# Kernel optimization log

Hardware: AMD Instinct MI355X
Metric: run time of the kernel (lower is better)

The kernel has to match this reference:

```python
import jax, jax.numpy as jnp
import numpy as np
from jax import lax

SOS_TOKEN = 0
PAD_LEN = 30  # tokenizer.pad_len -> number of greedy decode steps


def _gru_cell(x, h, w_ih, w_hh, b_ih, b_hh):
    # PyTorch GRU cell math. x,h: [B,H]; w_*: [3H,H]; b_*: [3H]
    gi = x @ w_ih.T + b_ih
    gh = h @ w_hh.T + b_hh
    i_r, i_z, i_n = jnp.split(gi, 3, axis=-1)
    h_r, h_z, h_n = jnp.split(gh, 3, axis=-1)
    r = jax.nn.sigmoid(i_r + h_r)
    z = jax.nn.sigmoid(i_z + h_z)
    n = jnp.tanh(i_n + r * h_n)
    return (1.0 - z) * n + z * h


def _sm_encode(sm_hidden, conv_w, conv_b, enc_w, enc_b):
    # sm_hidden: [B, L, C] -> conv over time with C input channels
    x = jnp.transpose(sm_hidden, (0, 2, 1))  # [B, C, L]
    conv = lax.conv_general_dilated(
        x, conv_w, window_strides=(1,), padding='VALID',
        dimension_numbers=('NCH', 'OIH', 'NCH'))  # [B, O, L-k+1]
    conv = jax.nn.relu(conv + conv_b[None, :, None])
    pooled = jnp.max(conv, axis=-1)  # [B, O]
    return jax.nn.relu(pooled @ enc_w.T + enc_b)  # [B, H]


def reference(sm_hidden, embedding, w_ih, w_hh, b_ih, b_hh,
              w_out, b_out, conv_w, conv_b, enc_w, enc_b):
    B = sm_hidden.shape[0]
    h0 = _sm_encode(sm_hidden, conv_w, conv_b, enc_w, enc_b)  # [B, H]

    # The original re-runs the GRU over the whole (append-only) prefix each
    # iteration; since the GRU is deterministic this equals incremental
    # single-step updates, which we do here.
    def step(carry, _):
        h, tok = carry
        emb = embedding[tok]                      # [B, H]
        h_new = _gru_cell(emb, h, w_ih, w_hh, b_ih, b_hh)
        logits = h_new @ w_out.T + b_out          # [B, V]
        tok_new = jnp.argmax(logits, axis=-1)     # greedy topk(1)
        return (h_new, tok_new), (h_new, tok_new)

    tok0 = jnp.full((B,), SOS_TOKEN, dtype=jnp.int32)
    (h_last, _), (hiddens, toks) = lax.scan(step, (h0, tok0), None, length=PAD_LEN)

    decoder_output = jax.nn.log_softmax(h_last @ w_out.T + b_out, axis=1)  # [B, V]
    decoder_hidden = hiddens  # [PAD_LEN, B, H] == rnn_out of final _base_forward
    decoded_indices = jnp.concatenate([tok0[None, :], toks], axis=0)  # [PAD_LEN+1, B]
    return decoder_output, decoder_hidden, decoded_indices


def setup_inputs() -> dict:
    key = jax.random.key(0)
    ks = jax.random.split(key, 12)
    B, L, C = 512, 120, 128
    H, V, O, K = 1024, 512, 32, 10
    s = 1.0 / np.sqrt(H)
    return {
        'sm_hidden': jax.random.normal(ks[0], (B, L, C), jnp.float32),
        'embedding': jax.random.normal(ks[1], (V, H), jnp.float32),
        'w_ih': jax.random.uniform(ks[2], (3 * H, H), jnp.float32, -s, s),
        'w_hh': jax.random.uniform(ks[3], (3 * H, H), jnp.float32, -s, s),
        'b_ih': jax.random.uniform(ks[4], (3 * H,), jnp.float32, -s, s),
        'b_hh': jax.random.uniform(ks[5], (3 * H,), jnp.float32, -s, s),
        'w_out': jax.random.uniform(ks[6], (V, H), jnp.float32, -s, s),
        'b_out': jax.random.uniform(ks[7], (V,), jnp.float32, -s, s),
        'conv_w': jax.random.normal(ks[8], (O, C, K), jnp.float32) * 0.05,
        'conv_b': jax.random.normal(ks[9], (O,), jnp.float32) * 0.05,
        'enc_w': jax.random.uniform(ks[10], (H, O), jnp.float32, -s, s),
        'enc_b': jax.random.uniform(ks[11], (H,), jnp.float32, -s, s),
    }
```

## Files before the change

kernel.cpp:

```cpp
#include <hip/hip_runtime.h>
#include <hip/hip_bf16.h>
#include <math.h>

#define Bsz 512
#define Hd 1024
#define Vd 512
#define Cc 128
#define Ll 120
#define Kk 10
#define Oo 32
#define NSTEP 30

typedef __attribute__((ext_vector_type(8))) short bf16x8;
typedef __attribute__((ext_vector_type(4))) float f32x4;
typedef unsigned short ushort;
typedef unsigned long long u64;

static __device__ __forceinline__ float sigm(float x) { return 1.f / (1.f + expf(-x)); }
static __device__ __forceinline__ ushort f2bf(float x) {
    __hip_bfloat16 h = __float2bfloat16(x);
    return *(ushort*)&h;
}
static __device__ __forceinline__ float bf2f(ushort u) {
    __hip_bfloat16 h; *(ushort*)&h = u;
    return __bfloat162float(h);
}
static __device__ __forceinline__ unsigned monofy(float f) {
    unsigned u = __float_as_uint(f);
    return (u & 0x80000000u) ? ~u : (u | 0x80000000u);
}

__global__ void k_split(const float* __restrict__ in, ushort* __restrict__ hi,
                        ushort* __restrict__ lo, int n) {
    int i = blockIdx.x * 256 + threadIdx.x;
    if (i < n) {
        float v = in[i];
        ushort h = f2bf(v);
        hi[i] = h;
        lo[i] = f2bf(v - bf2f(h));
    }
}

__global__ void k_pack(const float* __restrict__ W, ushort* __restrict__ hi,
                       ushort* __restrict__ lo, int total) {
    int idx = blockIdx.x * 256 + threadIdx.x;
    if (idx >= total) return;
    int jj = idx & 7, l = (idx >> 3) & 63, c = (idx >> 9) & 31, nf = idx >> 14;
    int n = nf * 16 + (l & 15);
    int k = c * 32 + ((l >> 4) << 3) + jj;
    float v = W[(size_t)n * 1024 + k];
    ushort h = f2bf(v);
    hi[idx] = h;
    lo[idx] = f2bf(v - bf2f(h));
}

__global__ void k_packconv(const float* __restrict__ cw, ushort* __restrict__ hi,
                           ushort* __restrict__ lo) {
    int idx = blockIdx.x * 256 + threadIdx.x;
    if (idx >= 2 * 40 * 64 * 8) return;
    int jj = idx & 7, l = (idx >> 3) & 63, ch = (idx >> 9) % 40, nf = idx / (40 * 512);
    int o = nf * 16 + (l & 15);
    int k = ch * 32 + ((l >> 4) << 3) + jj;
    int kc = k >> 7, c = k & 127;
    float v = cw[(o * Cc + c) * Kk + kc];
    ushort h = f2bf(v);
    hi[idx] = h;
    lo[idx] = f2bf(v - bf2f(h));
}

__global__ __launch_bounds__(256) void k_convmfma(const ushort* __restrict__ xH,
                                                  const ushort* __restrict__ xL,
                                                  const ushort* __restrict__ wH,
                                                  const ushort* __restrict__ wL,
                                                  const float* __restrict__ cb,
                                                  const float* __restrict__ ew,
                                                  const float* __restrict__ eb,
                                                  float* __restrict__ h0,
                                                  ushort* __restrict__ ApHi,
                                                  ushort* __restrict__ ApLo) {
    __shared__ float sred[4][2][16];
    __shared__ float ps[Oo];
    int tid = threadIdx.x, wid = tid >> 6, l = tid & 63;

    for (int b2 = 0; b2 < 2; ++b2) {
        int b = blockIdx.x * 2 + b2;
        f32x4 acc[2][2];
#pragma unroll
        for (int i = 0; i < 2; ++i)
#pragma unroll
            for (int j = 0; j < 2; ++j) acc[i][j] = (f32x4)0.f;

        bf16x8 aH0[2], aL0[2], bH0[2], bL0[2];
        bf16x8 aH1[2], aL1[2], bH1[2], bL1[2];

#define CLD(AH, AL, BH, BL, ch)                                                        \
    {                                                                                  \
        _Pragma("unroll") for (int tf2 = 0; tf2 < 2; ++tf2) {                          \
            int aoff = ((b * 120 + (wid * 2 + tf2) * 16 + (l & 15) + ((ch) >> 2)) * 128 \
                        + ((ch) & 3) * 32 + ((l >> 4) << 3));                          \
            AH[tf2] = *(const bf16x8*)(xH + aoff);                                     \
            AL[tf2] = *(const bf16x8*)(xL + aoff);                                     \
        }                                                                              \
        _Pragma("unroll") for (int nf = 0; nf < 2; ++nf) {                             \
            int boff = ((nf * 40 + (ch)) * 64 + l) * 8;                                \
            BH[nf] = *(const bf16x8*)(wH + boff);                                      \
            BL[nf] = *(const bf16x8*)(wL + boff);                                      \
        }                                                                              \
    }
#define CST(AH, AL, BH, BL)                                                            \
    {                                                                                  \
        _Pragma("unroll") for (int tf2 = 0; tf2 < 2; ++tf2)                            \
            _Pragma("unroll") for (int nf = 0; nf < 2; ++nf) {                         \
                acc[tf2][nf] = __builtin_amdgcn_mfma_f32_16x16x32_bf16(                \
                    AH[tf2], BH[nf], acc[tf2][nf], 0, 0, 0);                           \
                acc[tf2][nf] = __builtin_amdgcn_mfma_f32_16x16x32_bf16(                \
                    AH[tf2], BL[nf], acc[tf2][nf], 0, 0, 0);                           \
                acc[tf2][nf] = __builtin_amdgcn_mfma_f32_16x16x32_bf16(                \
                    AL[tf2], BH[nf], acc[tf2][nf], 0, 0, 0);                           \
            }                                                                          \
    }

        CLD(aH0, aL0, bH0, bL0, 0)
#pragma unroll
        for (int ch = 0; ch < 40; ch += 2) {
            CLD(aH1, aL1, bH1, bL1, ch + 1)
            CST(aH0, aL0, bH0, bL0)
            if (ch + 2 < 40) CLD(aH0, aL0, bH0, bL0, ch + 2)
            CST(aH1, aL1, bH1, bL1)
        }
#undef CLD
#undef CST

        float mx[2] = {-1e38f, -1e38f};
#pragma unroll
        for (int tf2 = 0; tf2 < 2; ++tf2) {
            int tb = (wid * 2 + tf2) * 16 + ((l >> 4) << 2);
#pragma unroll
            for (int q = 0; q < 4; ++q) {
                if (tb + q <= 110) {
                    mx[0] = fmaxf(mx[0], acc[tf2][0][q]);
                    mx[1] = fmaxf(mx[1], acc[tf2][1][q]);
                }
            }
        }
#pragma unroll
        for (int s = 16; s < 64; s <<= 1) {
            mx[0] = fmaxf(mx[0], __shfl_xor(mx[0], s));
            mx[1] = fmaxf(mx[1], __shfl_xor(mx[1], s));
        }
        if (l < 16) {
            sred[wid][0][l] = mx[0];
            sred[wid][1][l] = mx[1];
        }
        __syncthreads();
        if (tid < Oo) {
            float m = sred[0][tid >> 4][tid & 15];
#pragma unroll
            for (int w = 1; w < 4; ++w) m = fmaxf(m, sred[w][tid >> 4][tid & 15]);
            ps[tid] = fmaxf(m + cb[tid], 0.f);
        }
        __syncthreads();
        for (int j = tid; j < Hd; j += 256) {
            float a = eb[j];
            const float4* e4 = (const float4*)(ew + (size_t)j * Oo);
#pragma unroll
            for (int c4 = 0; c4 < 8; ++c4) {
                float4 w = e4[c4];
                a += ps[c4 * 4 + 0] * w.x + ps[c4 * 4 + 1] * w.y +
                     ps[c4 * 4 + 2] * w.z + ps[c4 * 4 + 3] * w.w;
            }
            a = fmaxf(a, 0.f);
            h0[(size_t)b * Hd + j] = a;
            ushort hb = f2bf(a);
            ushort lb = f2bf(a - bf2f(hb));
            int c = j >> 5, sub = (j >> 3) & 3, jj = j & 7, mf = b >> 4;
            int lane_r = (b & 15) + (sub << 4);
            int flat = ((mf * 32 + c) * 64 + lane_r) * 8 + jj;
            ApHi[flat] = hb;
            ApLo[flat] = lb;
        }
        __syncthreads();
    }
}

template <int EPI>
__global__ __launch_bounds__(512, 4) void k_rnn(const ushort* __restrict__ Ah,
                                                const ushort* __restrict__ Al,
                                                const ushort* __restrict__ Bh,
                                                const ushort* __restrict__ Bl,
                                                const float* __restrict__ bias,
                                                float* __restrict__ outF,
                                                const float* __restrict__ gi_all,
                                                const u64* __restrict__ pkRd,
                                                u64* __restrict__ pkWr,
                                                float* __restrict__ outIdxRow,
                                                const float* __restrict__ hOld,
                                                ushort* __restrict__ ApHi,
                                                ushort* __restrict__ ApLo) {
    __shared__ ushort Bs[2][24][512];
    int id = blockIdx.x;
    int xcd = id & 7, r = id >> 3;
    int jt = xcd * 4 + (r & 3);
    int mt = r >> 2;
    int tid = threadIdx.x, wid = tid >> 6, l = tid & 63;
    int wm = wid >> 1, wj = wid & 1;
    int mf = mt * 4 + wm;
    int jf = jt * 2 + wj;
    int jcol = jf * 16 + (l & 15);

    float giR[4][3], hR[4];
    int bR[4], tkR[4];
    if constexpr (EPI == 1) {
#pragma unroll
        for (int q = 0; q < 4; ++q) {
            bR[q] = mf * 16 + ((l >> 4) << 2) + q;
            u64 pk = pkRd[bR[q]];
            tkR[q] = 511 - (int)(unsigned)(pk & 0xFFFFFFFFu);
            const float* gi = gi_all + (size_t)tkR[q] * 3072;
            giR[q][0] = gi[jcol];
            giR[q][1] = gi[1024 + jcol];
            giR[q][2] = gi[2048 + jcol];
            hR[q] = hOld[(size_t)bR[q] * 1024 + jcol];
        }
        if (jt == 0 && wj == 0 && (l & 15) == 0) {
#pragma unroll
            for (int q = 0; q < 4; ++q) {
                pkWr[bR[q]] = 0ULL;
                if (outIdxRow) outIdxRow[bR[q]] = (float)tkR[q];
            }
        }
    }

    f32x4 acc[3];
#pragma unroll
    for (int g = 0; g < 3; ++g) acc[g] = (f32x4)0.f;

    bf16x8 stg[3], aH0[2], aL0[2], aH1[2], aL1[2];

#define STG_LD(it)                                                                     \
    {                                                                                  \
        _Pragma("unroll") for (int k = 0; k < 3; ++k) {                                \
            int u = wid + 8 * k;                                                       \
            int hl = u & 1, wjb = (u >> 1) & 1, g = (u >> 2) % 3, cu = u / 12;         \
            const ushort* sp = hl ? Bl : Bh;                                           \
            stg[k] = *(const bf16x8*)(sp +                                             \
                (size_t)(((g * 64 + jt * 2 + wjb) * 32 + (it) * 2 + cu) * 64 + l) * 8);\
        }                                                                              \
    }
#define STG_WR(buf)                                                                    \
    {                                                                                  \
        _Pragma("unroll") for (int k = 0; k < 3; ++k)                                  \
            *(bf16x8*)&Bs[buf][wid + 8 * k][l * 8] = stg[k];                           \
    }
#define A_LD(DH, DL, it)                                                               \
    {                                                                                  \
        _Pragma("unroll") for (int cc = 0; cc < 2; ++cc) {                             \
            DH[cc] = *(const bf16x8*)(Ah + (size_t)((mf * 32 + (it) * 2 + cc) * 64 + l) * 8); \
            DL[cc] = *(const bf16x8*)(Al + (size_t)((mf * 32 + (it) * 2 + cc) * 64 + l) * 8); \
        }                                                                              \
    }
#define CMP(buf, AH, AL)                                                               \
    {                                                                                  \
        _Pragma("unroll") for (int cc = 0; cc < 2; ++cc)                               \
            _Pragma("unroll") for (int g = 0; g < 3; ++g) {                            \
                bf16x8 bhh = *(const bf16x8*)&Bs[buf][cc * 12 + g * 4 + wj * 2 + 0][l * 8]; \
                bf16x8 bll = *(const bf16x8*)&Bs[buf][cc * 12 + g * 4 + wj * 2 + 1][l * 8]; \
                acc[g] = __builtin_amdgcn_mfma_f32_16x16x32_bf16(AH[cc], bhh, acc[g], 0, 0, 0); \
                acc[g] = __builtin_amdgcn_mfma_f32_16x16x32_bf16(AH[cc], bll, acc[g], 0, 0, 0); \
                acc[g] = __builtin_amdgcn_mfma_f32_16x16x32_bf16(AL[cc], bhh, acc[g], 0, 0, 0); \
            }                                                                          \
    }

    STG_LD(0)
    STG_WR(0)
    STG_LD(1)
    A_LD(aH0, aL0, 0)
    __syncthreads();
#pragma unroll
    for (int it = 0; it < 16; ++it) {
        int buf = it & 1;
        if (it < 15) STG_WR(buf ^ 1)
        if (it < 14) STG_LD(it + 2)
        if (it & 1) {
            if (it < 15) A_LD(aH0, aL0, it + 1)
            CMP(buf, aH1, aL1)
        } else {
            if (it < 15) A_LD(aH1, aL1, it + 1)
            CMP(buf, aH0, aL0)
        }
        __syncthreads();
    }
#undef STG_LD
#undef STG_WR
#undef A_LD
#undef CMP

    if constexpr (EPI == 0) {
#pragma unroll
        for (int q = 0; q < 4; ++q) {
            int b = mf * 16 + ((l >> 4) << 2) + q;
#pragma unroll
            for (int g = 0; g < 3; ++g)
                outF[(size_t)b * 3072 + g * 1024 + jcol] =
                    acc[g][q] + bias[g * 1024 + jcol];
        }
    } else {
        float bj0 = bias[jcol], bj1 = bias[1024 + jcol], bj2 = bias[2048 + jcol];
        int c = jcol >> 5, sub = (jcol >> 3) & 3, jj = jcol & 7;
#pragma unroll
        for (int q = 0; q < 4; ++q) {
            int b = bR[q];
            float rr = sigm(giR[q][0] + acc[0][q] + bj0);
            float zz = sigm(giR[q][1] + acc[1][q] + bj1);
            float nn = tanhf(giR[q][2] + rr * (acc[2][q] + bj2));
            float hv = (1.f - zz) * nn + zz * hR[q];
            outF[(size_t)b * 1024 + jcol] = hv;
            ushort hb = f2bf(hv);
            ushort lb = f2bf(hv - bf2f(hb));
            int lane_r = (b & 15) + (sub << 4);
            int flat = ((mf * 32 + c) * 64 + lane_r) * 8 + jj;
            ApHi[flat] = hb;
            ApLo[flat] = lb;
        }
    }
}

__global__ __launch_bounds__(256) void k_lgt(const ushort* __restrict__ Ah,
                                             const ushort* __restrict__ Al,
                                             const ushort* __restrict__ Bh,
                                             const ushort* __restrict__ Bl,
                                             const float* __restrict__ bias,
                                             float* __restrict__ outF,
                                             u64* __restrict__ pkOut) {
    int p = blockIdx.x * 4 + (threadIdx.x >> 6);
    int l = threadIdx.x & 63;
    int mf = p >> 5, vf = p & 31;
    size_t ab = (size_t)(mf * 32) * 512 + l * 8;
    size_t bb = (size_t)(vf * 32) * 512 + l * 8;
    f32x4 acc = (f32x4)0.f;
    bf16x8 a0h, a0l, b0h, b0l, a1h, a1l, b1h, b1l;

#define LD1(AH, AL, BH, BL, c)                                                         \
    {                                                                                  \
        AH = *(const bf16x8*)(Ah + ab + (size_t)(c) * 512);                            \
        AL = *(const bf16x8*)(Al + ab + (size_t)(c) * 512);                            \
        BH = *(const bf16x8*)(Bh + bb + (size_t)(c) * 512);                            \
        BL = *(const bf16x8*)(Bl + bb + (size_t)(c) * 512);                            \
    }
#define ST1(AH, AL, BH, BL)                                                            \
    {                                                                                  \
        acc = __builtin_amdgcn_mfma_f32_16x16x32_bf16(AH, BH, acc, 0, 0, 0);           \
        acc = __builtin_amdgcn_mfma_f32_16x16x32_bf16(AH, BL, acc, 0, 0, 0);           \
        acc = __builtin_amdgcn_mfma_f32_16x16x32_bf16(AL, BH, acc, 0, 0, 0);           \
    }

    LD1(a0h, a0l, b0h, b0l, 0)
#pragma unroll
    for (int c = 0; c < 32; c += 2) {
        LD1(a1h, a1l, b1h, b1l, c + 1)
        ST1(a0h, a0l, b0h, b0l)
        if (c + 2 < 32) LD1(a0h, a0l, b0h, b0l, c + 2)
        ST1(a1h, a1l, b1h, b1l)
    }
#undef LD1
#undef ST1

    int v = vf * 16 + (l & 15);
    float bv = bias[v];
    float lg[4];
    unsigned vmq[4];
#pragma unroll
    for (int q = 0; q < 4; ++q) {
        int b = mf * 16 + ((l >> 4) << 2) + q;
        lg[q] = acc[q] + bv;
        outF[(size_t)b * Vd + v] = lg[q];
        vmq[q] = 511u - (unsigned)v;
    }
#pragma unroll
    for (int off = 1; off < 16; off <<= 1) {
#pragma unroll
        for (int q = 0; q < 4; ++q) {
            float og = __shfl_xor(lg[q], off);
            unsigned ov = __shfl_xor(vmq[q], off);
            if (og > lg[q] || (og == lg[q] && ov > vmq[q])) { lg[q] = og; vmq[q] = ov; }
        }
    }
    if ((l & 15) == 0) {
#pragma unroll
        for (int q = 0; q < 4; ++q) {
            int b = mf * 16 + ((l >> 4) << 2) + q;
            u64 pk = ((u64)monofy(lg[q]) << 32) | (u64)vmq[q];
            atomicMax(&pkOut[b], pk);
        }
    }
}

__global__ __launch_bounds__(64) void k_fin(const float* __restrict__ logits,
                                            const u64* __restrict__ pk,
                                            float* __restrict__ out_lsm,
                                            float* __restrict__ outIdxRow) {
    int b = blockIdx.x, l = threadIdx.x;
    const float* row = logits + (size_t)b * Vd;
    float bv = -3.4e38f;
#pragma unroll
    for (int s = 0; s < 8; ++s) bv = fmaxf(bv, row[s * 64 + l]);
#pragma unroll
    for (int off = 1; off < 64; off <<= 1) bv = fmaxf(bv, __shfl_xor(bv, off));
    float sum = 0.f;
#pragma unroll
    for (int s = 0; s < 8; ++s) sum += expf(row[s * 64 + l] - bv);
#pragma unroll
    for (int off = 1; off < 64; off <<= 1) sum += __shfl_xor(sum, off);
    float lse = logf(sum) + bv;
#pragma unroll
    for (int s = 0; s < 8; ++s) {
        int v = s * 64 + l;
        out_lsm[(size_t)b * Vd + v] = row[v] - lse;
    }
    if (l == 0)
        outIdxRow[b] = (float)(511 - (int)(unsigned)(pk[b] & 0xFFFFFFFFu));
}

__global__ void k_init(u64* __restrict__ P0, float* __restrict__ out_idx0) {
    int i = blockIdx.x * 64 + threadIdx.x;
    if (i < Bsz) {
        P0[i] = (1ULL << 32) | 511ULL;
        out_idx0[i] = 0.f;
    }
}

extern "C" void kernel_launch(void* const* d_in, const int* in_sizes, int n_in,
                              void* d_out, int out_size, void* d_ws, size_t ws_size,
                              hipStream_t stream) {
    const float* sm    = (const float*)d_in[0];
    const float* emb   = (const float*)d_in[1];
    const float* w_ih  = (const float*)d_in[2];
    const float* w_hh  = (const float*)d_in[3];
    const float* b_ih  = (const float*)d_in[4];
    const float* b_hh  = (const float*)d_in[5];
    const float* w_out = (const float*)d_in[6];
    const float* b_out = (const float*)d_in[7];
    const float* cw    = (const float*)d_in[8];
    const float* cb    = (const float*)d_in[9];
    const float* ew    = (const float*)d_in[10];
    const float* eb    = (const float*)d_in[11];

    float* out0 = (float*)d_out;
    float* out1 = out0 + (size_t)Bsz * Vd;
    float* out2 = out1 + (size_t)NSTEP * Bsz * Hd;

    const int SMN = Bsz * Ll * Cc;
    char* wsp = (char*)d_ws;
    float*  f_gi  = (float*)wsp;  wsp += sizeof(float) * Bsz * 3072;
    float*  f_h0  = (float*)wsp;  wsp += sizeof(float) * Bsz * Hd;
    float*  f_log = (float*)wsp;  wsp += sizeof(float) * Bsz * Vd;
    u64*    Ppk0  = (u64*)wsp;    wsp += sizeof(u64) * Bsz;
    u64*    Ppk1  = (u64*)wsp;    wsp += sizeof(u64) * Bsz;
    ushort* ApHi0 = (ushort*)wsp; wsp += sizeof(ushort) * Bsz * Hd;
    ushort* ApLo0 = (ushort*)wsp; wsp += sizeof(ushort) * Bsz * Hd;
    ushort* ApHi1 = (ushort*)wsp; wsp += sizeof(ushort) * Bsz * Hd;
    ushort* ApLo1 = (ushort*)wsp; wsp += sizeof(ushort) * Bsz * Hd;
    ushort* embH  = (ushort*)wsp; wsp += sizeof(ushort) * Vd * Hd;
    ushort* embL  = (ushort*)wsp; wsp += sizeof(ushort) * Vd * Hd;
    ushort* wihH  = (ushort*)wsp; wsp += sizeof(ushort) * 3072 * Hd;
    ushort* wihL  = (ushort*)wsp; wsp += sizeof(ushort) * 3072 * Hd;
    ushort* whhH  = (ushort*)wsp; wsp += sizeof(ushort) * 3072 * Hd;
    ushort* whhL  = (ushort*)wsp; wsp += sizeof(ushort) * 3072 * Hd;
    ushort* woutH = (ushort*)wsp; wsp += sizeof(ushort) * Vd * Hd;
    ushort* woutL = (ushort*)wsp; wsp += sizeof(ushort) * Vd * Hd;
    ushort* smH   = (ushort*)wsp; wsp += sizeof(ushort) * (SMN + 32 * Cc);
    ushort* smL   = (ushort*)wsp; wsp += sizeof(ushort) * (SMN + 32 * Cc);
    ushort* cwBH  = (ushort*)wsp; wsp += sizeof(ushort) * 2 * 40 * 64 * 8;
    ushort* cwBL  = (ushort*)wsp; wsp += sizeof(ushort) * 2 * 40 * 64 * 8;

    k_split<<<SMN / 256, 256, 0, stream>>>(sm, smH, smL, SMN);
    k_packconv<<<160, 256, 0, stream>>>(cw, cwBH, cwBL);
    k_pack<<<(3072 * 1024) / 256, 256, 0, stream>>>(w_ih, wihH, wihL, 3072 * 1024);
    k_pack<<<(3072 * 1024) / 256, 256, 0, stream>>>(w_hh, whhH, whhL, 3072 * 1024);
    k_pack<<<(512 * 1024) / 256, 256, 0, stream>>>(w_out, woutH, woutL, 512 * 1024);
    k_pack<<<(512 * 1024) / 256, 256, 0, stream>>>(emb, embH, embL, 512 * 1024);
    k_convmfma<<<256, 256, 0, stream>>>(smH, smL, cwBH, cwBL, cb, ew, eb,
                                        f_h0, ApHi0, ApLo0);
    k_rnn<0><<<256, 512, 0, stream>>>(embH, embL, wihH, wihL, b_ih, f_gi,
                                      nullptr, nullptr, nullptr, nullptr, nullptr,
                                      nullptr, nullptr);
    k_init<<<8, 64, 0, stream>>>(Ppk0, out2);

    ushort* aH[2] = {ApHi0, ApHi1};
    ushort* aL[2] = {ApLo0, ApLo1};
    u64* P[2] = {Ppk0, Ppk1};
    for (int t = 0; t < NSTEP; ++t) {
        int cur = t & 1, nxt = cur ^ 1;
        const float* hOld = (t == 0) ? f_h0 : (out1 + (size_t)(t - 1) * Bsz * Hd);
        k_rnn<1><<<256, 512, 0, stream>>>(
            aH[cur], aL[cur], whhH, whhL, b_hh, out1 + (size_t)t * Bsz * Hd,
            f_gi, P[t & 1], P[(t + 1) & 1],
            (t >= 1) ? (out2 + (size_t)t * Bsz) : nullptr,
            hOld, aH[nxt], aL[nxt]);
        k_lgt<<<256, 256, 0, stream>>>(aH[nxt], aL[nxt], woutH, woutL, b_out,
                                       f_log, P[(t + 1) & 1]);
    }
    k_fin<<<Bsz, 64, 0, stream>>>(f_log, P[NSTEP & 1], out0,
                                  out2 + (size_t)NSTEP * Bsz);
}
```

Measured before the change: 926.6 us.

## Split recurrent GEMM into split-K partial kernel plus fused reduce-epilogue kernel

The per-step recurrent GEMM (h @ w_hh) is now a split-K kernel. Each block keeps its whole w_hh tile in LDS and covers all 512 batch rows over a quarter of K, so weights are loaded once per block and not re-streamed per batch tile. A separate reduce kernel sums the four partials and applies the GRU gate epilogue, argmax-token gather and bf16 split. The input-gate GEMM gets its own kernel with a deeper K chunk per iteration, and the conv encoder uses one block per batch row. This trades an extra launch and a 4x partial buffer round-trip through global memory for better weight reuse and parallelism.

```diff
diff --git a/kernel.cpp b/kernel.cpp
--- a/kernel.cpp
+++ b/kernel.cpp
@@ -80,18 +80,15 @@
                                                   ushort* __restrict__ ApLo) {
     __shared__ float sred[4][2][16];
     __shared__ float ps[Oo];
-    int tid = threadIdx.x, wid = tid >> 6, l = tid & 63;
-
-    for (int b2 = 0; b2 < 2; ++b2) {
-        int b = blockIdx.x * 2 + b2;
-        f32x4 acc[2][2];
-#pragma unroll
-        for (int i = 0; i < 2; ++i)
-#pragma unroll
-            for (int j = 0; j < 2; ++j) acc[i][j] = (f32x4)0.f;
-
-        bf16x8 aH0[2], aL0[2], bH0[2], bL0[2];
-        bf16x8 aH1[2], aL1[2], bH1[2], bL1[2];
+    int b = blockIdx.x, tid = threadIdx.x, wid = tid >> 6, l = tid & 63;
+    f32x4 acc[2][2];
+#pragma unroll
+    for (int i = 0; i < 2; ++i)
+#pragma unroll
+        for (int j = 0; j < 2; ++j) acc[i][j] = (f32x4)0.f;
+
+    bf16x8 aH0[2], aL0[2], bH0[2], bL0[2];
+    bf16x8 aH1[2], aL1[2], bH1[2], bL1[2];
 
 #define CLD(AH, AL, BH, BL, ch)                                                        \
     {                                                                                  \
@@ -120,84 +117,74 @@
             }                                                                          \
     }
 
-        CLD(aH0, aL0, bH0, bL0, 0)
-#pragma unroll
-        for (int ch = 0; ch < 40; ch += 2) {
-            CLD(aH1, aL1, bH1, bL1, ch + 1)
-            CST(aH0, aL0, bH0, bL0)
-            if (ch + 2 < 40) CLD(aH0, aL0, bH0, bL0, ch + 2)
-            CST(aH1, aL1, bH1, bL1)
-        }
+    CLD(aH0, aL0, bH0, bL0, 0)
+#pragma unroll
+    for (int ch = 0; ch < 40; ch += 2) {
+        CLD(aH1, aL1, bH1, bL1, ch + 1)
+        CST(aH0, aL0, bH0, bL0)
+        if (ch + 2 < 40) CLD(aH0, aL0, bH0, bL0, ch + 2)
+        CST(aH1, aL1, bH1, bL1)
+    }
 #undef CLD
 #undef CST
 
-        float mx[2] = {-1e38f, -1e38f};
-#pragma unroll
-        for (int tf2 = 0; tf2 < 2; ++tf2) {
-            int tb = (wid * 2 + tf2) * 16 + ((l >> 4) << 2);
-#pragma unroll
-            for (int q = 0; q < 4; ++q) {
-                if (tb + q <= 110) {
-                    mx[0] = fmaxf(mx[0], acc[tf2][0][q]);
-                    mx[1] = fmaxf(mx[1], acc[tf2][1][q]);
-                }
+    float mx[2] = {-1e38f, -1e38f};
+#pragma unroll
+    for (int tf2 = 0; tf2 < 2; ++tf2) {
+        int tb = (wid * 2 + tf2) * 16 + ((l >> 4) << 2);
+#pragma unroll
+        for (int q = 0; q < 4; ++q) {
+            if (tb + q <= 110) {
+                mx[0] = fmaxf(mx[0], acc[tf2][0][q]);
+                mx[1] = fmaxf(mx[1], acc[tf2][1][q]);
             }
         }
-#pragma unroll
-        for (int s = 16; s < 64; s <<= 1) {
-            mx[0] = fmaxf(mx[0], __shfl_xor(mx[0], s));
-            mx[1] = fmaxf(mx[1], __shfl_xor(mx[1], s));
-        }
-        if (l < 16) {
-            sred[wid][0][l] = mx[0];
-            sred[wid][1][l] = mx[1];
-        }
-        __syncthreads();
-        if (tid < Oo) {
-            float m = sred[0][tid >> 4][tid & 15];
-#pragma unroll
-            for (int w = 1; w < 4; ++w) m = fmaxf(m, sred[w][tid >> 4][tid & 15]);
-            ps[tid] = fmaxf(m + cb[tid], 0.f);
-        }
-        __syncthreads();
-        for (int j = tid; j < Hd; j += 256) {
-            float a = eb[j];
-            const float4* e4 = (const float4*)(ew + (size_t)j * Oo);
-#pragma unroll
-            for (int c4 = 0; c4 < 8; ++c4) {
-                float4 w = e4[c4];
-                a += ps[c4 * 4 + 0] * w.x + ps[c4 * 4 + 1] * w.y +
-                     ps[c4 * 4 + 2] * w.z + ps[c4 * 4 + 3] * w.w;
-            }
-            a = fmaxf(a, 0.f);
-            h0[(size_t)b * Hd + j] = a;
-            ushort hb = f2bf(a);
-            ushort lb = f2bf(a - bf2f(hb));
-            int c = j >> 5, sub = (j >> 3) & 3, jj = j & 7, mf = b >> 4;
-            int lane_r = (b & 15) + (sub << 4);
-            int flat = ((mf * 32 + c) * 64 + lane_r) * 8 + jj;
-            ApHi[flat] = hb;
-            ApLo[flat] = lb;
-        }
-        __syncthreads();
-    }
-}
-
-template <int EPI>
-__global__ __launch_bounds__(512, 4) void k_rnn(const ushort* __restrict__ Ah,
-                                                const ushort* __restrict__ Al,
-                                                const ushort* __restrict__ Bh,
-                                                const ushort* __restrict__ Bl,
-                                                const float* __restrict__ bias,
-                                                float* __restrict__ outF,
-                                                const float* __restrict__ gi_all,
-                                                const u64* __restrict__ pkRd,
-                                                u64* __restrict__ pkWr,
-                                                float* __restrict__ outIdxRow,
-                                                const float* __restrict__ hOld,
-                                                ushort* __restrict__ ApHi,
-                                                ushort* __restrict__ ApLo) {
-    __shared__ ushort Bs[2][24][512];
+    }
+#pragma unroll
+    for (int s = 16; s < 64; s <<= 1) {
+        mx[0] = fmaxf(mx[0], __shfl_xor(mx[0], s));
+        mx[1] = fmaxf(mx[1], __shfl_xor(mx[1], s));
+    }
+    if (l < 16) {
+        sred[wid][0][l] = mx[0];
+        sred[wid][1][l] = mx[1];
+    }
+    __syncthreads();
+    if (tid < Oo) {
+        float m = sred[0][tid >> 4][tid & 15];
+#pragma unroll
+        for (int w = 1; w < 4; ++w) m = fmaxf(m, sred[w][tid >> 4][tid & 15]);
+        ps[tid] = fmaxf(m + cb[tid], 0.f);
+    }
+    __syncthreads();
+    for (int j = tid; j < Hd; j += 256) {
+        float a = eb[j];
+        const float4* e4 = (const float4*)(ew + (size_t)j * Oo);
+#pragma unroll
+        for (int c4 = 0; c4 < 8; ++c4) {
+            float4 w = e4[c4];
+            a += ps[c4 * 4 + 0] * w.x + ps[c4 * 4 + 1] * w.y +
+                 ps[c4 * 4 + 2] * w.z + ps[c4 * 4 + 3] * w.w;
+        }
+        a = fmaxf(a, 0.f);
+        h0[(size_t)b * Hd + j] = a;
+        ushort hb = f2bf(a);
+        ushort lb = f2bf(a - bf2f(hb));
+        int c = j >> 5, sub = (j >> 3) & 3, jj = j & 7, mf = b >> 4;
+        int lane_r = (b & 15) + (sub << 4);
+        int flat = ((mf * 32 + c) * 64 + lane_r) * 8 + jj;
+        ApHi[flat] = hb;
+        ApLo[flat] = lb;
+    }
+}
+
+__global__ __launch_bounds__(512, 2) void k_gi(const ushort* __restrict__ Ah,
+                                               const ushort* __restrict__ Al,
+                                               const ushort* __restrict__ Bh,
+                                               const ushort* __restrict__ Bl,
+                                               const float* __restrict__ bias,
+                                               float* __restrict__ outF) {
+    __shared__ ushort Bs[2][48][512];
     int id = blockIdx.x;
     int xcd = id & 7, r = id >> 3;
     int jt = xcd * 4 + (r & 3);
@@ -208,60 +195,37 @@
     int jf = jt * 2 + wj;
     int jcol = jf * 16 + (l & 15);
 
-    float giR[4][3], hR[4];
-    int bR[4], tkR[4];
-    if constexpr (EPI == 1) {
-#pragma unroll
-        for (int q = 0; q < 4; ++q) {
-            bR[q] = mf * 16 + ((l >> 4) << 2) + q;
-            u64 pk = pkRd[bR[q]];
-            tkR[q] = 511 - (int)(unsigned)(pk & 0xFFFFFFFFu);
-            const float* gi = gi_all + (size_t)tkR[q] * 3072;
-            giR[q][0] = gi[jcol];
-            giR[q][1] = gi[1024 + jcol];
-            giR[q][2] = gi[2048 + jcol];
-            hR[q] = hOld[(size_t)bR[q] * 1024 + jcol];
-        }
-        if (jt == 0 && wj == 0 && (l & 15) == 0) {
-#pragma unroll
-            for (int q = 0; q < 4; ++q) {
-                pkWr[bR[q]] = 0ULL;
-                if (outIdxRow) outIdxRow[bR[q]] = (float)tkR[q];
-            }
-        }
-    }
-
     f32x4 acc[3];
 #pragma unroll
     for (int g = 0; g < 3; ++g) acc[g] = (f32x4)0.f;
 
-    bf16x8 stg[3], aH0[2], aL0[2], aH1[2], aL1[2];
+    bf16x8 stg[6], aH0[4], aL0[4], aH1[4], aL1[4];
 
 #define STG_LD(it)                                                                     \
     {                                                                                  \
-        _Pragma("unroll") for (int k = 0; k < 3; ++k) {                                \
+        _Pragma("unroll") for (int k = 0; k < 6; ++k) {                                \
             int u = wid + 8 * k;                                                       \
             int hl = u & 1, wjb = (u >> 1) & 1, g = (u >> 2) % 3, cu = u / 12;         \
             const ushort* sp = hl ? Bl : Bh;                                           \
             stg[k] = *(const bf16x8*)(sp +                                             \
-                (size_t)(((g * 64 + jt * 2 + wjb) * 32 + (it) * 2 + cu) * 64 + l) * 8);\
+                (size_t)(((g * 64 + jt * 2 + wjb) * 32 + (it) * 4 + cu) * 64 + l) * 8);\
         }                                                                              \
     }
 #define STG_WR(buf)                                                                    \
     {                                                                                  \
-        _Pragma("unroll") for (int k = 0; k < 3; ++k)                                  \
+        _Pragma("unroll") for (int k = 0; k < 6; ++k)                                  \
             *(bf16x8*)&Bs[buf][wid + 8 * k][l * 8] = stg[k];                           \
     }
 #define A_LD(DH, DL, it)                                                               \
     {                                                                                  \
-        _Pragma("unroll") for (int cc = 0; cc < 2; ++cc) {                             \
-            DH[cc] = *(const bf16x8*)(Ah + (size_t)((mf * 32 + (it) * 2 + cc) * 64 + l) * 8); \
-            DL[cc] = *(const bf16x8*)(Al + (size_t)((mf * 32 + (it) * 2 + cc) * 64 + l) * 8); \
+        _Pragma("unroll") for (int cc = 0; cc < 4; ++cc) {                             \
+            DH[cc] = *(const bf16x8*)(Ah + (size_t)((mf * 32 + (it) * 4 + cc) * 64 + l) * 8); \
+            DL[cc] = *(const bf16x8*)(Al + (size_t)((mf * 32 + (it) * 4 + cc) * 64 + l) * 8); \
         }                                                                              \
     }
 #define CMP(buf, AH, AL)                                                               \
     {                                                                                  \
-        _Pragma("unroll") for (int cc = 0; cc < 2; ++cc)                               \
+        _Pragma("unroll") for (int cc = 0; cc < 4; ++cc)                               \
             _Pragma("unroll") for (int g = 0; g < 3; ++g) {                            \
                 bf16x8 bhh = *(const bf16x8*)&Bs[buf][cc * 12 + g * 4 + wj * 2 + 0][l * 8]; \
                 bf16x8 bll = *(const bf16x8*)&Bs[buf][cc * 12 + g * 4 + wj * 2 + 1][l * 8]; \
@@ -277,15 +241,15 @@
     A_LD(aH0, aL0, 0)
     __syncthreads();
 #pragma unroll
-    for (int it = 0; it < 16; ++it) {
+    for (int it = 0; it < 8; ++it) {
         int buf = it & 1;
-        if (it < 15) STG_WR(buf ^ 1)
-        if (it < 14) STG_LD(it + 2)
+        if (it < 7) STG_WR(buf ^ 1)
+        if (it < 6) STG_LD(it + 2)
         if (it & 1) {
-            if (it < 15) A_LD(aH0, aL0, it + 1)
+            if (it < 7) A_LD(aH0, aL0, it + 1)
             CMP(buf, aH1, aL1)
         } else {
-            if (it < 15) A_LD(aH1, aL1, it + 1)
+            if (it < 7) A_LD(aH1, aL1, it + 1)
             CMP(buf, aH0, aL0)
         }
         __syncthreads();
@@ -295,32 +259,149 @@
 #undef A_LD
 #undef CMP
 
-    if constexpr (EPI == 0) {
-#pragma unroll
-        for (int q = 0; q < 4; ++q) {
-            int b = mf * 16 + ((l >> 4) << 2) + q;
-#pragma unroll
-            for (int g = 0; g < 3; ++g)
-                outF[(size_t)b * 3072 + g * 1024 + jcol] =
-                    acc[g][q] + bias[g * 1024 + jcol];
-        }
-    } else {
-        float bj0 = bias[jcol], bj1 = bias[1024 + jcol], bj2 = bias[2048 + jcol];
-        int c = jcol >> 5, sub = (jcol >> 3) & 3, jj = jcol & 7;
-#pragma unroll
-        for (int q = 0; q < 4; ++q) {
-            int b = bR[q];
-            float rr = sigm(giR[q][0] + acc[0][q] + bj0);
-            float zz = sigm(giR[q][1] + acc[1][q] + bj1);
-            float nn = tanhf(giR[q][2] + rr * (acc[2][q] + bj2));
-            float hv = (1.f - zz) * nn + zz * hR[q];
-            outF[(size_t)b * 1024 + jcol] = hv;
-            ushort hb = f2bf(hv);
-            ushort lb = f2bf(hv - bf2f(hb));
-            int lane_r = (b & 15) + (sub << 4);
-            int flat = ((mf * 32 + c) * 64 + lane_r) * 8 + jj;
-            ApHi[flat] = hb;
-            ApLo[flat] = lb;
+#pragma unroll
+    for (int q = 0; q < 4; ++q) {
+        int b = mf * 16 + ((l >> 4) << 2) + q;
+#pragma unroll
+        for (int g = 0; g < 3; ++g)
+            outF[(size_t)b * 3072 + g * 1024 + jcol] = acc[g][q] + bias[g * 1024 + jcol];
+    }
+}
+
+__global__ __launch_bounds__(512, 2) void k_rgemm(const ushort* __restrict__ Ah,
+                                                  const ushort* __restrict__ Al,
+                                                  const ushort* __restrict__ Bh,
+                                                  const ushort* __restrict__ Bl,
+                                                  float* __restrict__ part) {
+    __shared__ ushort Bs[8 * 6 * 512];
+    int id = blockIdx.x;
+    int xcd = id & 7, slot = id >> 3;
+    int jt = xcd * 8 + (slot & 7);
+    int ks = slot >> 3;
+    int tid = threadIdx.x, wm = tid >> 6, l = tid & 63;
+
+#pragma unroll
+    for (int k = 0; k < 6; ++k) {
+        int i = tid + 512 * k;
+        int il = i & 63, u = i >> 6;
+        int chunk = u / 6, unit = u - chunk * 6;
+        int g = unit >> 1, hl = unit & 1;
+        const ushort* sp = hl ? Bl : Bh;
+        bf16x8 v = *(const bf16x8*)(sp +
+            (size_t)(((g * 64 + jt) * 32 + ks * 8 + chunk) * 64 + il) * 8);
+        *(bf16x8*)&Bs[(size_t)i * 8] = v;
+    }
+
+    f32x4 acc[3][4];
+#pragma unroll
+    for (int g = 0; g < 3; ++g)
+#pragma unroll
+        for (int m = 0; m < 4; ++m) acc[g][m] = (f32x4)0.f;
+
+    bf16x8 a0h[4], a0l[4], a1h[4], a1l[4];
+#define ALD(DH, DL, ch)                                                                \
+    {                                                                                  \
+        _Pragma("unroll") for (int m = 0; m < 4; ++m) {                                \
+            size_t off = (size_t)(((wm * 4 + m) * 32 + ks * 8 + (ch)) * 64 + l) * 8;   \
+            DH[m] = *(const bf16x8*)(Ah + off);                                        \
+            DL[m] = *(const bf16x8*)(Al + off);                                        \
+        }                                                                              \
+    }
+    ALD(a0h, a0l, 0)
+    ALD(a1h, a1l, 1)
+    __syncthreads();
+
+#pragma unroll
+    for (int ch = 0; ch < 8; ++ch) {
+#pragma unroll
+        for (int g = 0; g < 3; ++g) {
+            bf16x8 bh = *(const bf16x8*)&Bs[((ch * 6 + g * 2 + 0) * 64 + l) * 8];
+            bf16x8 bl = *(const bf16x8*)&Bs[((ch * 6 + g * 2 + 1) * 64 + l) * 8];
+            if (ch & 1) {
+#pragma unroll
+                for (int m = 0; m < 4; ++m) {
+                    acc[g][m] = __builtin_amdgcn_mfma_f32_16x16x32_bf16(a1h[m], bh, acc[g][m], 0, 0, 0);
+                    acc[g][m] = __builtin_amdgcn_mfma_f32_16x16x32_bf16(a1h[m], bl, acc[g][m], 0, 0, 0);
+                    acc[g][m] = __builtin_amdgcn_mfma_f32_16x16x32_bf16(a1l[m], bh, acc[g][m], 0, 0, 0);
+                }
+            } else {
+#pragma unroll
+                for (int m = 0; m < 4; ++m) {
+                    acc[g][m] = __builtin_amdgcn_mfma_f32_16x16x32_bf16(a0h[m], bh, acc[g][m], 0, 0, 0);
+                    acc[g][m] = __builtin_amdgcn_mfma_f32_16x16x32_bf16(a0h[m], bl, acc[g][m], 0, 0, 0);
+                    acc[g][m] = __builtin_amdgcn_mfma_f32_16x16x32_bf16(a0l[m], bh, acc[g][m], 0, 0, 0);
+                }
+            }
+        }
+        if (ch < 6) {
+            if (ch & 1) { ALD(a1h, a1l, ch + 2) }
+            else        { ALD(a0h, a0l, ch + 2) }
+        }
+    }
+#undef ALD
+
+#pragma unroll
+    for (int g = 0; g < 3; ++g)
+#pragma unroll
+        for (int m = 0; m < 4; ++m)
+#pragma unroll
+            for (int q = 0; q < 4; ++q) {
+                int b = wm * 64 + m * 16 + ((l >> 4) << 2) + q;
+                part[(size_t)(ks * 512 + b) * 3072 + g * 1024 + jt * 16 + (l & 15)] =
+                    acc[g][m][q];
+            }
+}
+
+__global__ __launch_bounds__(256) void k_rred(const float* __restrict__ part,
+                                              const float* __restrict__ bias,
+                                              const float* __restrict__ gi_all,
+                                              const u64* __restrict__ pkRd,
+                                              u64* __restrict__ pkWr,
+                                              float* __restrict__ outIdxRow,
+                                              const float* __restrict__ hOld,
+                                              float* __restrict__ outH,
+                                              ushort* __restrict__ ApHi,
+                                              ushort* __restrict__ ApLo) {
+    int id = blockIdx.x;
+    int xcd = id & 7, slot = id >> 3;
+    int jt = xcd * 8 + (slot >> 3);
+    int bgrp = slot & 7;
+    int tid = threadIdx.x, tj = tid & 15, tb = tid >> 4;
+    int jcol = jt * 16 + tj;
+    float bj0 = bias[jcol], bj1 = bias[1024 + jcol], bj2 = bias[2048 + jcol];
+    int c = jcol >> 5, sub = (jcol >> 3) & 3, jj = jcol & 7;
+
+#pragma unroll
+    for (int bb = 0; bb < 4; ++bb) {
+        int b = bgrp * 64 + bb * 16 + tb;
+        u64 pk = pkRd[b];
+        int tk = 511 - (int)(unsigned)(pk & 0xFFFFFFFFu);
+        const float* gi = gi_all + (size_t)tk * 3072;
+        float gh[3];
+#pragma unroll
+        for (int g = 0; g < 3; ++g) {
+            size_t base = (size_t)b * 3072 + g * 1024 + jcol;
+            float s = part[base];
+            s += part[(size_t)1 * 512 * 3072 + base];
+            s += part[(size_t)2 * 512 * 3072 + base];
+            s += part[(size_t)3 * 512 * 3072 + base];
+            gh[g] = s;
+        }
+        float rr = sigm(gi[jcol] + gh[0] + bj0);
+        float zz = sigm(gi[1024 + jcol] + gh[1] + bj1);
+        float nn = tanhf(gi[2048 + jcol] + rr * (gh[2] + bj2));
+        float hv = (1.f - zz) * nn + zz * hOld[(size_t)b * 1024 + jcol];
+        outH[(size_t)b * 1024 + jcol] = hv;
+        ushort hb = f2bf(hv);
+        ushort lb = f2bf(hv - bf2f(hb));
+        int mf = b >> 4;
+        int lane_r = (b & 15) + (sub << 4);
+        int flat = ((mf * 32 + c) * 64 + lane_r) * 8 + jj;
+        ApHi[flat] = hb;
+        ApLo[flat] = lb;
+        if (jt == 0 && tj == 0) {
+            pkWr[b] = 0ULL;
+            if (outIdxRow) outIdxRow[b] = (float)tk;
         }
     }
 }
@@ -451,6 +532,7 @@
 
     const int SMN = Bsz * Ll * Cc;
     char* wsp = (char*)d_ws;
+    float*  f_part = (float*)wsp; wsp += sizeof(float) * 4 * Bsz * 3072;
     float*  f_gi  = (float*)wsp;  wsp += sizeof(float) * Bsz * 3072;
     float*  f_h0  = (float*)wsp;  wsp += sizeof(float) * Bsz * Hd;
     float*  f_log = (float*)wsp;  wsp += sizeof(float) * Bsz * Vd;
@@ -479,11 +561,9 @@
     k_pack<<<(3072 * 1024) / 256, 256, 0, stream>>>(w_hh, whhH, whhL, 3072 * 1024);
     k_pack<<<(512 * 1024) / 256, 256, 0, stream>>>(w_out, woutH, woutL, 512 * 1024);
     k_pack<<<(512 * 1024) / 256, 256, 0, stream>>>(emb, embH, embL, 512 * 1024);
-    k_convmfma<<<256, 256, 0, stream>>>(smH, smL, cwBH, cwBL, cb, ew, eb,
+    k_convmfma<<<Bsz, 256, 0, stream>>>(smH, smL, cwBH, cwBL, cb, ew, eb,
                                         f_h0, ApHi0, ApLo0);
-    k_rnn<0><<<256, 512, 0, stream>>>(embH, embL, wihH, wihL, b_ih, f_gi,
-                                      nullptr, nullptr, nullptr, nullptr, nullptr,
-                                      nullptr, nullptr);
+    k_gi<<<256, 512, 0, stream>>>(embH, embL, wihH, wihL, b_ih, f_gi);
     k_init<<<8, 64, 0, stream>>>(Ppk0, out2);
 
     ushort* aH[2] = {ApHi0, ApHi1};
@@ -492,11 +572,11 @@
     for (int t = 0; t < NSTEP; ++t) {
         int cur = t & 1, nxt = cur ^ 1;
         const float* hOld = (t == 0) ? f_h0 : (out1 + (size_t)(t - 1) * Bsz * Hd);
-        k_rnn<1><<<256, 512, 0, stream>>>(
-            aH[cur], aL[cur], whhH, whhL, b_hh, out1 + (size_t)t * Bsz * Hd,
-            f_gi, P[t & 1], P[(t + 1) & 1],
-            (t >= 1) ? (out2 + (size_t)t * Bsz) : nullptr,
-            hOld, aH[nxt], aL[nxt]);
+        k_rgemm<<<256, 512, 0, stream>>>(aH[cur], aL[cur], whhH, whhL, f_part);
+        k_rred<<<512, 256, 0, stream>>>(f_part, b_hh, f_gi, P[t & 1], P[(t + 1) & 1],
+                                        (t >= 1) ? (out2 + (size_t)t * Bsz) : nullptr,
+                                        hOld, out1 + (size_t)t * Bsz * Hd,
+                                        aH[nxt], aL[nxt]);
         k_lgt<<<256, 256, 0, stream>>>(aH[nxt], aL[nxt], woutH, woutL, b_out,
                                        f_log, P[(t + 1) & 1]);
     }
```

After: 1.165 ms. 1.26x slower.

## Fuse input bf16 split into conv kernel via swizzled LDS; deepen RNN K-chunks

Applied to the files above, without the earlier changes.

The separate k_split pass over the 31 MB sequence input is removed. The conv kernel now loads fp32 rows directly, splits them into hi/lo bf16 in XOR-swizzled shared memory, and runs one batch row per block (512 blocks). The goal is to avoid writing and re-reading the split copy through global memory. Separately, k_rnn doubles its K-chunk per iteration (48-row LDS stage, 8 iterations instead of 16) and relaxes launch bounds to 2 blocks per CU. That trades occupancy for fewer barriers and more loads in flight per iteration.

```diff
diff --git a/kernel.cpp b/kernel.cpp
--- a/kernel.cpp
+++ b/kernel.cpp
@@ -28,17 +28,6 @@
 static __device__ __forceinline__ unsigned monofy(float f) {
     unsigned u = __float_as_uint(f);
     return (u & 0x80000000u) ? ~u : (u | 0x80000000u);
-}
-
-__global__ void k_split(const float* __restrict__ in, ushort* __restrict__ hi,
-                        ushort* __restrict__ lo, int n) {
-    int i = blockIdx.x * 256 + threadIdx.x;
-    if (i < n) {
-        float v = in[i];
-        ushort h = f2bf(v);
-        hi[i] = h;
-        lo[i] = f2bf(v - bf2f(h));
-    }
 }
 
 __global__ void k_pack(const float* __restrict__ W, ushort* __restrict__ hi,
@@ -68,8 +57,7 @@
     lo[idx] = f2bf(v - bf2f(h));
 }
 
-__global__ __launch_bounds__(256) void k_convmfma(const ushort* __restrict__ xH,
-                                                  const ushort* __restrict__ xL,
+__global__ __launch_bounds__(256) void k_convmfma(const float* __restrict__ sm,
                                                   const ushort* __restrict__ wH,
                                                   const ushort* __restrict__ wL,
                                                   const float* __restrict__ cb,
@@ -78,28 +66,48 @@
                                                   float* __restrict__ h0,
                                                   ushort* __restrict__ ApHi,
                                                   ushort* __restrict__ ApLo) {
+    __shared__ ushort hiS[137 * 128];
+    __shared__ ushort loS[137 * 128];
     __shared__ float sred[4][2][16];
     __shared__ float ps[Oo];
-    int tid = threadIdx.x, wid = tid >> 6, l = tid & 63;
-
-    for (int b2 = 0; b2 < 2; ++b2) {
-        int b = blockIdx.x * 2 + b2;
-        f32x4 acc[2][2];
-#pragma unroll
-        for (int i = 0; i < 2; ++i)
-#pragma unroll
-            for (int j = 0; j < 2; ++j) acc[i][j] = (f32x4)0.f;
-
-        bf16x8 aH0[2], aL0[2], bH0[2], bL0[2];
-        bf16x8 aH1[2], aL1[2], bH1[2], bL1[2];
+    int b = blockIdx.x, tid = threadIdx.x, wid = tid >> 6, l = tid & 63;
+
+    const float* smb = sm + (size_t)b * (Ll * Cc);
+    for (int i = tid; i < 1920; i += 256) {
+        int row = i >> 4, col0 = (i & 15) * 8;
+        float4 fa = *(const float4*)(smb + row * Cc + col0);
+        float4 fb = *(const float4*)(smb + row * Cc + col0 + 4);
+        float vv[8] = {fa.x, fa.y, fa.z, fa.w, fb.x, fb.y, fb.z, fb.w};
+        ushort h8[8], l8[8];
+#pragma unroll
+        for (int q = 0; q < 8; ++q) {
+            ushort h = f2bf(vv[q]);
+            h8[q] = h;
+            l8[q] = f2bf(vv[q] - bf2f(h));
+        }
+        int o = ((row << 8) + (col0 << 1)) ^ ((row & 7) << 4);
+        *(bf16x8*)((char*)hiS + o) = *(bf16x8*)h8;
+        *(bf16x8*)((char*)loS + o) = *(bf16x8*)l8;
+    }
+    __syncthreads();
+
+    f32x4 acc[2][2];
+#pragma unroll
+    for (int i = 0; i < 2; ++i)
+#pragma unroll
+        for (int j = 0; j < 2; ++j) acc[i][j] = (f32x4)0.f;
+
+    bf16x8 aH0[2], aL0[2], bH0[2], bL0[2];
+    bf16x8 aH1[2], aL1[2], bH1[2], bL1[2];
 
 #define CLD(AH, AL, BH, BL, ch)                                                        \
     {                                                                                  \
         _Pragma("unroll") for (int tf2 = 0; tf2 < 2; ++tf2) {                          \
-            int aoff = ((b * 120 + (wid * 2 + tf2) * 16 + (l & 15) + ((ch) >> 2)) * 128 \
-                        + ((ch) & 3) * 32 + ((l >> 4) << 3));                          \
-            AH[tf2] = *(const bf16x8*)(xH + aoff);                                     \
-            AL[tf2] = *(const bf16x8*)(xL + aoff);                                     \
+            int row = (wid * 2 + tf2) * 16 + (l & 15) + ((ch) >> 2);                   \
+            int o = ((row << 8) + ((((ch) & 3) * 32 + ((l >> 4) << 3)) << 1))          \
+                    ^ ((row & 7) << 4);                                                \
+            AH[tf2] = *(const bf16x8*)((const char*)hiS + o);                          \
+            AL[tf2] = *(const bf16x8*)((const char*)loS + o);                          \
         }                                                                              \
         _Pragma("unroll") for (int nf = 0; nf < 2; ++nf) {                             \
             int boff = ((nf * 40 + (ch)) * 64 + l) * 8;                                \
@@ -120,71 +128,69 @@
             }                                                                          \
     }
 
-        CLD(aH0, aL0, bH0, bL0, 0)
-#pragma unroll
-        for (int ch = 0; ch < 40; ch += 2) {
-            CLD(aH1, aL1, bH1, bL1, ch + 1)
-            CST(aH0, aL0, bH0, bL0)
-            if (ch + 2 < 40) CLD(aH0, aL0, bH0, bL0, ch + 2)
-            CST(aH1, aL1, bH1, bL1)
-        }
+    CLD(aH0, aL0, bH0, bL0, 0)
+#pragma unroll
+    for (int ch = 0; ch < 40; ch += 2) {
+        CLD(aH1, aL1, bH1, bL1, ch + 1)
+        CST(aH0, aL0, bH0, bL0)
+        if (ch + 2 < 40) CLD(aH0, aL0, bH0, bL0, ch + 2)
+        CST(aH1, aL1, bH1, bL1)
+    }
 #undef CLD
 #undef CST
 
-        float mx[2] = {-1e38f, -1e38f};
-#pragma unroll
-        for (int tf2 = 0; tf2 < 2; ++tf2) {
-            int tb = (wid * 2 + tf2) * 16 + ((l >> 4) << 2);
-#pragma unroll
-            for (int q = 0; q < 4; ++q) {
-                if (tb + q <= 110) {
-                    mx[0] = fmaxf(mx[0], acc[tf2][0][q]);
-                    mx[1] = fmaxf(mx[1], acc[tf2][1][q]);
-                }
+    float mx[2] = {-1e38f, -1e38f};
+#pragma unroll
+    for (int tf2 = 0; tf2 < 2; ++tf2) {
+        int tb = (wid * 2 + tf2) * 16 + ((l >> 4) << 2);
+#pragma unroll
+        for (int q = 0; q < 4; ++q) {
+            if (tb + q <= 110) {
+                mx[0] = fmaxf(mx[0], acc[tf2][0][q]);
+                mx[1] = fmaxf(mx[1], acc[tf2][1][q]);
             }
         }
-#pragma unroll
-        for (int s = 16; s < 64; s <<= 1) {
-            mx[0] = fmaxf(mx[0], __shfl_xor(mx[0], s));
-            mx[1] = fmaxf(mx[1], __shfl_xor(mx[1], s));
-        }
-        if (l < 16) {
-            sred[wid][0][l] = mx[0];
-            sred[wid][1][l] = mx[1];
-        }
-        __syncthreads();
-        if (tid < Oo) {
-            float m = sred[0][tid >> 4][tid & 15];
-#pragma unroll
-            for (int w = 1; w < 4; ++w) m = fmaxf(m, sred[w][tid >> 4][tid & 15]);
-            ps[tid] = fmaxf(m + cb[tid], 0.f);
-        }
-        __syncthreads();
-        for (int j = tid; j < Hd; j += 256) {
-            float a = eb[j];
-            const float4* e4 = (const float4*)(ew + (size_t)j * Oo);
-#pragma unroll
-            for (int c4 = 0; c4 < 8; ++c4) {
-                float4 w = e4[c4];
-                a += ps[c4 * 4 + 0] * w.x + ps[c4 * 4 + 1] * w.y +
-                     ps[c4 * 4 + 2] * w.z + ps[c4 * 4 + 3] * w.w;
-            }
-            a = fmaxf(a, 0.f);
-            h0[(size_t)b * Hd + j] = a;
-            ushort hb = f2bf(a);
-            ushort lb = f2bf(a - bf2f(hb));
-            int c = j >> 5, sub = (j >> 3) & 3, jj = j & 7, mf = b >> 4;
-            int lane_r = (b & 15) + (sub << 4);
-            int flat = ((mf * 32 + c) * 64 + lane_r) * 8 + jj;
-            ApHi[flat] = hb;
-            ApLo[flat] = lb;
-        }
-        __syncthreads();
+    }
+#pragma unroll
+    for (int s = 16; s < 64; s <<= 1) {
+        mx[0] = fmaxf(mx[0], __shfl_xor(mx[0], s));
+        mx[1] = fmaxf(mx[1], __shfl_xor(mx[1], s));
+    }
+    if (l < 16) {
+        sred[wid][0][l] = mx[0];
+        sred[wid][1][l] = mx[1];
+    }
+    __syncthreads();
+    if (tid < Oo) {
+        float m = sred[0][tid >> 4][tid & 15];
+#pragma unroll
+        for (int w = 1; w < 4; ++w) m = fmaxf(m, sred[w][tid >> 4][tid & 15]);
+        ps[tid] = fmaxf(m + cb[tid], 0.f);
+    }
+    __syncthreads();
+    for (int j = tid; j < Hd; j += 256) {
+        float a = eb[j];
+        const float4* e4 = (const float4*)(ew + (size_t)j * Oo);
+#pragma unroll
+        for (int c4 = 0; c4 < 8; ++c4) {
+            float4 w = e4[c4];
+            a += ps[c4 * 4 + 0] * w.x + ps[c4 * 4 + 1] * w.y +
+                 ps[c4 * 4 + 2] * w.z + ps[c4 * 4 + 3] * w.w;
+        }
+        a = fmaxf(a, 0.f);
+        h0[(size_t)b * Hd + j] = a;
+        ushort hb = f2bf(a);
+        ushort lb = f2bf(a - bf2f(hb));
+        int c = j >> 5, sub = (j >> 3) & 3, jj = j & 7, amf = b >> 4;
+        int lane_r = (b & 15) + (sub << 4);
+        int flat = ((amf * 32 + c) * 64 + lane_r) * 8 + jj;
+        ApHi[flat] = hb;
+        ApLo[flat] = lb;
     }
 }
 
 template <int EPI>
-__global__ __launch_bounds__(512, 4) void k_rnn(const ushort* __restrict__ Ah,
+__global__ __launch_bounds__(512, 2) void k_rnn(const ushort* __restrict__ Ah,
                                                 const ushort* __restrict__ Al,
                                                 const ushort* __restrict__ Bh,
                                                 const ushort* __restrict__ Bl,
@@ -197,7 +203,7 @@
                                                 const float* __restrict__ hOld,
                                                 ushort* __restrict__ ApHi,
                                                 ushort* __restrict__ ApLo) {
-    __shared__ ushort Bs[2][24][512];
+    __shared__ ushort Bs[2][48][512];
     int id = blockIdx.x;
     int xcd = id & 7, r = id >> 3;
     int jt = xcd * 4 + (r & 3);
@@ -235,33 +241,33 @@
 #pragma unroll
     for (int g = 0; g < 3; ++g) acc[g] = (f32x4)0.f;
 
-    bf16x8 stg[3], aH0[2], aL0[2], aH1[2], aL1[2];
+    bf16x8 stg[6], aH0[4], aL0[4], aH1[4], aL1[4];
 
 #define STG_LD(it)                                                                     \
     {                                                                                  \
-        _Pragma("unroll") for (int k = 0; k < 3; ++k) {                                \
+        _Pragma("unroll") for (int k = 0; k < 6; ++k) {                                \
             int u = wid + 8 * k;                                                       \
             int hl = u & 1, wjb = (u >> 1) & 1, g = (u >> 2) % 3, cu = u / 12;         \
             const ushort* sp = hl ? Bl : Bh;                                           \
             stg[k] = *(const bf16x8*)(sp +                                             \
-                (size_t)(((g * 64 + jt * 2 + wjb) * 32 + (it) * 2 + cu) * 64 + l) * 8);\
+                (size_t)(((g * 64 + jt * 2 + wjb) * 32 + (it) * 4 + cu) * 64 + l) * 8);\
         }                                                                              \
     }
 #define STG_WR(buf)                                                                    \
     {                                                                                  \
-        _Pragma("unroll") for (int k = 0; k < 3; ++k)                                  \
+        _Pragma("unroll") for (int k = 0; k < 6; ++k)                                  \
             *(bf16x8*)&Bs[buf][wid + 8 * k][l * 8] = stg[k];                           \
     }
 #define A_LD(DH, DL, it)                                                               \
     {                                                                                  \
-        _Pragma("unroll") for (int cc = 0; cc < 2; ++cc) {                             \
-            DH[cc] = *(const bf16x8*)(Ah + (size_t)((mf * 32 + (it) * 2 + cc) * 64 + l) * 8); \
-            DL[cc] = *(const bf16x8*)(Al + (size_t)((mf * 32 + (it) * 2 + cc) * 64 + l) * 8); \
+        _Pragma("unroll") for (int cc = 0; cc < 4; ++cc) {                             \
+            DH[cc] = *(const bf16x8*)(Ah + (size_t)((mf * 32 + (it) * 4 + cc) * 64 + l) * 8); \
+            DL[cc] = *(const bf16x8*)(Al + (size_t)((mf * 32 + (it) * 4 + cc) * 64 + l) * 8); \
         }                                                                              \
     }
 #define CMP(buf, AH, AL)                                                               \
     {                                                                                  \
-        _Pragma("unroll") for (int cc = 0; cc < 2; ++cc)                               \
+        _Pragma("unroll") for (int cc = 0; cc < 4; ++cc)                               \
             _Pragma("unroll") for (int g = 0; g < 3; ++g) {                            \
                 bf16x8 bhh = *(const bf16x8*)&Bs[buf][cc * 12 + g * 4 + wj * 2 + 0][l * 8]; \
                 bf16x8 bll = *(const bf16x8*)&Bs[buf][cc * 12 + g * 4 + wj * 2 + 1][l * 8]; \
@@ -277,15 +283,15 @@
     A_LD(aH0, aL0, 0)
     __syncthreads();
 #pragma unroll
-    for (int it = 0; it < 16; ++it) {
+    for (int it = 0; it < 8; ++it) {
         int buf = it & 1;
-        if (it < 15) STG_WR(buf ^ 1)
-        if (it < 14) STG_LD(it + 2)
+        if (it < 7) STG_WR(buf ^ 1)
+        if (it < 6) STG_LD(it + 2)
         if (it & 1) {
-            if (it < 15) A_LD(aH0, aL0, it + 1)
+            if (it < 7) A_LD(aH0, aL0, it + 1)
             CMP(buf, aH1, aL1)
         } else {
-            if (it < 15) A_LD(aH1, aL1, it + 1)
+            if (it < 7) A_LD(aH1, aL1, it + 1)
             CMP(buf, aH0, aL0)
         }
         __syncthreads();
@@ -318,7 +324,7 @@
             ushort hb = f2bf(hv);
             ushort lb = f2bf(hv - bf2f(hb));
             int lane_r = (b & 15) + (sub << 4);
-            int flat = ((mf * 32 + c) * 64 + lane_r) * 8 + jj;
+            int flat = (((b >> 4) * 32 + c) * 64 + lane_r) * 8 + jj;
             ApHi[flat] = hb;
             ApLo[flat] = lb;
         }
@@ -449,7 +455,6 @@
     float* out1 = out0 + (size_t)Bsz * Vd;
     float* out2 = out1 + (size_t)NSTEP * Bsz * Hd;
 
-    const int SMN = Bsz * Ll * Cc;
     char* wsp = (char*)d_ws;
     float*  f_gi  = (float*)wsp;  wsp += sizeof(float) * Bsz * 3072;
     float*  f_h0  = (float*)wsp;  wsp += sizeof(float) * Bsz * Hd;
@@ -468,18 +473,15 @@
     ushort* whhL  = (ushort*)wsp; wsp += sizeof(ushort) * 3072 * Hd;
     ushort* woutH = (ushort*)wsp; wsp += sizeof(ushort) * Vd * Hd;
     ushort* woutL = (ushort*)wsp; wsp += sizeof(ushort) * Vd * Hd;
-    ushort* smH   = (ushort*)wsp; wsp += sizeof(ushort) * (SMN + 32 * Cc);
-    ushort* smL   = (ushort*)wsp; wsp += sizeof(ushort) * (SMN + 32 * Cc);
     ushort* cwBH  = (ushort*)wsp; wsp += sizeof(ushort) * 2 * 40 * 64 * 8;
     ushort* cwBL  = (ushort*)wsp; wsp += sizeof(ushort) * 2 * 40 * 64 * 8;
 
-    k_split<<<SMN / 256, 256, 0, stream>>>(sm, smH, smL, SMN);
     k_packconv<<<160, 256, 0, stream>>>(cw, cwBH, cwBL);
     k_pack<<<(3072 * 1024) / 256, 256, 0, stream>>>(w_ih, wihH, wihL, 3072 * 1024);
     k_pack<<<(3072 * 1024) / 256, 256, 0, stream>>>(w_hh, whhH, whhL, 3072 * 1024);
     k_pack<<<(512 * 1024) / 256, 256, 0, stream>>>(w_out, woutH, woutL, 512 * 1024);
     k_pack<<<(512 * 1024) / 256, 256, 0, stream>>>(emb, embH, embL, 512 * 1024);
-    k_convmfma<<<256, 256, 0, stream>>>(smH, smL, cwBH, cwBL, cb, ew, eb,
+    k_convmfma<<<Bsz, 256, 0, stream>>>(sm, cwBH, cwBL, cb, ew, eb,
                                         f_h0, ApHi0, ApLo0);
     k_rnn<0><<<256, 512, 0, stream>>>(embH, embL, wihH, wihL, b_ih, f_gi,
                                       nullptr, nullptr, nullptr, nullptr, nullptr,
```

Measured after the change: 835.9 us. 9.8% less time.
